# Performance work log

Hardware: AMD Instinct MI355X
Metric: run time of the kernel (lower is better)

## Reference

```python
import jax, jax.numpy as jnp
import numpy as np

B_, C_, H_, W_, Dd_ = 2, 64, 32, 32, 32
D_INNER, D_STATE, DT_RANK, D_CONV = 64, 8, 4, 4


def setup_inputs() -> dict:
    key = jax.random.key(0)
    ks = jax.random.split(key, 12)
    s = 0.05
    A_init = jnp.log(jnp.tile(jnp.arange(1, D_STATE + 1, dtype=jnp.float32), (D_INNER, 1)))
    return {
        "input": jax.random.normal(ks[0], (B_, C_, H_, W_, Dd_), jnp.float32),
        "conv_w": jax.random.normal(ks[1], (C_, C_, 3, 3, 3), jnp.float32) * s,
        "conv_b": jax.random.normal(ks[2], (C_,), jnp.float32) * s,
        "in_proj_w": jax.random.normal(ks[3], (2 * D_INNER, C_), jnp.float32) * s,
        "conv1d_w": jax.random.normal(ks[4], (D_INNER, 1, D_CONV), jnp.float32) * s,
        "conv1d_b": jax.random.normal(ks[5], (D_INNER,), jnp.float32) * s,
        "x_proj_w": jax.random.normal(ks[6], (DT_RANK + 2 * D_STATE, D_INNER), jnp.float32) * s,
        "dt_proj_w": jax.random.normal(ks[7], (D_INNER, DT_RANK), jnp.float32) * s,
        "dt_proj_b": jax.random.normal(ks[8], (D_INNER,), jnp.float32) * s,
        "A_log": A_init,
        "A_b_log": A_init + 0.01,
        "D_skip": jnp.ones((D_INNER,), jnp.float32),
        "out_proj_w": jax.random.normal(ks[9], (C_, D_INNER), jnp.float32) * s,
        "ln_g": jnp.ones((C_,), jnp.float32),
        "ln_b": jnp.zeros((C_,), jnp.float32),
    }


def _conv3d(x, w, b):
    y = jax.lax.conv_general_dilated(x, w, (1, 1, 1), [(1, 1), (1, 1), (1, 1)],
                                     dimension_numbers=("NCDHW", "OIDHW", "NCDHW"))
    return y + b[None, :, None, None, None]


def _instance_norm(x, eps=1e-5):
    m = x.mean(axis=(2, 3, 4), keepdims=True)
    v = ((x - m) ** 2).mean(axis=(2, 3, 4), keepdims=True)
    return (x - m) * jax.lax.rsqrt(v + eps)


def _selective_scan(xc, dt, Bm, Cm, A, D_skip):
    # xc, dt: (b,L,d); Bm, Cm: (b,L,n); A: (d,n)
    dA = jnp.exp(dt[..., None] * A)                       # (b,L,d,n)
    dBx = (dt * xc)[..., None] * Bm[:, :, None, :]        # (b,L,d,n)

    def comb(l, r):
        al, bl = l
        ar, br = r
        return ar * al, ar * bl + br

    _, h = jax.lax.associative_scan(comb, (dA, dBx), axis=1)
    y = jnp.einsum("bldn,bln->bld", h, Cm)
    return y + xc * D_skip


def _direction(xz, conv1d_w, conv1d_b, x_proj_w, dt_proj_w, dt_proj_b, A, D_skip):
    x, z = jnp.split(xz, 2, axis=-1)                      # each (b,L,d)
    xt = jnp.swapaxes(x, 1, 2)                            # (b,d,L)
    xc = jax.lax.conv_general_dilated(xt, conv1d_w, (1,), [(D_CONV - 1, 0)],
                                      feature_group_count=D_INNER,
                                      dimension_numbers=("NCH", "OIH", "NCH"))
    xc = jax.nn.silu(jnp.swapaxes(xc + conv1d_b[None, :, None], 1, 2))  # (b,L,d)
    dbl = xc @ x_proj_w.T
    dt_r = dbl[..., :DT_RANK]
    Bm = dbl[..., DT_RANK:DT_RANK + D_STATE]
    Cm = dbl[..., DT_RANK + D_STATE:]
    dt = jax.nn.softplus(dt_r @ dt_proj_w.T + dt_proj_b)
    y = _selective_scan(xc, dt, Bm, Cm, A, D_skip)
    return y * jax.nn.silu(z)


def reference(input, conv_w, conv_b, in_proj_w, conv1d_w, conv1d_b, x_proj_w,
              dt_proj_w, dt_proj_b, A_log, A_b_log, D_skip, out_proj_w, ln_g, ln_b):
    # skip path: Conv3d -> InstanceNorm3d -> ReLU
    skip = jax.nn.relu(_instance_norm(_conv3d(input, conv_w, conv_b)))
    b, c, h, w, d = input.shape
    tokens = input.transpose(0, 2, 3, 4, 1).reshape(b, h * w * d, c)  # b (hwd) c
    xz = tokens @ in_proj_w.T                                          # (b,L,2d)
    A = -jnp.exp(A_log)
    A_b = -jnp.exp(A_b_log)
    y_f = _direction(xz, conv1d_w, conv1d_b, x_proj_w, dt_proj_w, dt_proj_b, A, D_skip)
    y_b = _direction(xz[:, ::-1], conv1d_w, conv1d_b, x_proj_w, dt_proj_w, dt_proj_b, A_b, D_skip)[:, ::-1]
    out = ((y_f + y_b) @ out_proj_w.T) / 2.0  # if_devide_out=True
    mu = out.mean(-1, keepdims=True)
    var = ((out - mu) ** 2).mean(-1, keepdims=True)
    out = (out - mu) * jax.lax.rsqrt(var + 1e-5) * ln_g + ln_b  # use_norm=True
    vol = out.reshape(b, h, w, d, c).transpose(0, 4, 1, 2, 3)
    return _conv3d(vol, conv_w, conv_b) + skip
```

## Files before the change

### kernel.cpp

```cpp
#include <hip/hip_runtime.h>
#include <hip/hip_bf16.h>

typedef __hip_bfloat16 bf16;
typedef __attribute__((ext_vector_type(8))) short short8;
typedef __attribute__((ext_vector_type(4))) float f32x4;

__device__ __forceinline__ float b2f(bf16 x){ return __bfloat162float(x); }
__device__ __forceinline__ bf16  f2b(float x){ return __float2bfloat16(x); }
__device__ __forceinline__ float s2f(short s){ bf16 t = *(bf16*)&s; return b2f(t); }

__device__ __forceinline__ float ldin(const void* p, size_t i, int f32){
  return f32 ? ((const float*)p)[i] : b2f(((const bf16*)p)[i]);
}
__device__ __forceinline__ void stout(void* p, size_t i, float v, int f32){
  if(f32) ((float*)p)[i] = v; else ((bf16*)p)[i] = f2b(v);
}

constexpr int SP   = 32*32*32;
constexpr int LTOK = SP;
constexpr int NC   = 512;
constexpr int CLEN = LTOK / NC;
constexpr int NSEQ = 2*2*64*8;
constexpr int SEG  = 16;
constexpr int SEGLEN = NC/SEG;

__global__ void k_detect(const void* conv_w, int* flag){
  if(threadIdx.x==0 && blockIdx.x==0){
    const bf16* p = (const bf16*)conv_w;
    int f = 0;
    for(int i=0;i<128;i++){
      float v = b2f(p[i]);
      if(!(v==v) || fabsf(v) > 1.0f) f = 1;
    }
    *flag = f;
  }
}

__global__ void k_fill(void* out, int n, const int* flag){
  const int f32 = *flag;
  int i = blockIdx.x*256 + threadIdx.x;
  if(i<n) stout(out, i, 12345.0f, f32);
}

__global__ void k_wprep(const void* __restrict__ cw, bf16* __restrict__ wt,
                        const int* __restrict__ flag){
  const int f32 = *flag;
  int t = blockIdx.x*256 + threadIdx.x;
  if(t >= 27*64*64) return;
  int tap = t >> 12;
  int oc  = (t >> 6) & 63;
  int ci  = t & 63;
  wt[t] = f2b(ldin(cw, ((size_t)(oc*64+ci))*27 + tap, f32));
}

__global__ __launch_bounds__(256) void k_inprojm(
    const void* __restrict__ in, const void* __restrict__ pw,
    bf16* __restrict__ xz, bf16* __restrict__ xin_t,
    const int* __restrict__ flag){
  const int f32 = *flag;
  __shared__ bf16 tok[128*72];
  __shared__ bf16 wl [128*72];
  int tid = threadIdx.x;
  int b = blockIdx.x >> 8, tile = blockIdx.x & 255;
  int l0 = tile*128;

  for(int p=tid; p<1024; p+=256){
    int j = p & 127, c8 = p >> 7;
    short8 v;
    #pragma unroll
    for(int k=0;k<8;k++){
      bf16 t = f2b(ldin(pw, j*64 + c8*8 + k, f32));
      v[k] = *(short*)&t;
    }
    *(short8*)(&wl[j*72 + c8*8]) = v;
  }
  for(int p=tid; p<1024; p+=256){
    int i = p & 127, c8 = p >> 7;
    short8 v;
    #pragma unroll
    for(int k=0;k<8;k++){
      bf16 t = f2b(ldin(in, ((size_t)(b*64 + c8*8 + k))*SP + l0 + i, f32));
      v[k] = *(short*)&t;
    }
    *(short8*)(&tok[i*72 + c8*8]) = v;
  }
  __syncthreads();

  int lane = tid & 63, wv = tid >> 6;
  int pn = lane & 15, quad = lane >> 4, kg8 = quad*8;
  f32x4 acc[2][8];
  #pragma unroll
  for(int mt=0;mt<2;mt++)
    #pragma unroll
    for(int nt=0;nt<8;nt++) acc[mt][nt]=(f32x4)(0.f);

  #pragma unroll
  for(int kq=0;kq<2;kq++){
    short8 a0 = *(const short8*)(&tok[(wv*32      + pn)*72 + kq*32 + kg8]);
    short8 a1 = *(const short8*)(&tok[(wv*32 + 16 + pn)*72 + kq*32 + kg8]);
    #pragma unroll
    for(int nt=0;nt<8;nt++){
      short8 bb = *(const short8*)(&wl[(nt*16+pn)*72 + kq*32 + kg8]);
      acc[0][nt] = __builtin_amdgcn_mfma_f32_16x16x32_bf16(a0,bb,acc[0][nt],0,0,0);
      acc[1][nt] = __builtin_amdgcn_mfma_f32_16x16x32_bf16(a1,bb,acc[1][nt],0,0,0);
    }
  }

  #pragma unroll
  for(int mt=0;mt<2;mt++){
    #pragma unroll
    for(int nt=0;nt<8;nt++){
      #pragma unroll
      for(int r=0;r<4;r++){
        int token = wv*32 + mt*16 + quad*4 + r;
        xz[((size_t)b*LTOK + l0 + token)*128 + nt*16 + pn] = f2b(acc[mt][nt][r]);
      }
    }
  }
  for(int p=tid; p<8192; p+=256){
    int i = p >> 6, c = p & 63;
    xin_t[((size_t)b*SP + l0 + i)*64 + c] = tok[i*72 + c];
  }
}

__global__ __launch_bounds__(256, 2) void k_convm(
    const bf16* __restrict__ xin_t, const bf16* __restrict__ wt,
    const void* __restrict__ cb, const bf16* __restrict__ skip,
    bf16* __restrict__ out_bf, void* __restrict__ out_any,
    int mode, const int* __restrict__ flag){
  const int f32 = *flag;
  __shared__ bf16 xt[612*44];

  int tid  = threadIdx.x;
  int lane = tid & 63;
  int wv   = tid >> 6;
  int pn   = lane & 15;
  int quad = lane >> 4;
  int kg8  = quad * 8;
  int laneA = pn*64 + kg8;

  int blk = blockIdx.x;
  int b  = blk >> 8;
  int h  = (blk >> 3) & 31;
  int w0 = (blk & 7) * 4;

  f32x4 acc[4][2];
  #pragma unroll
  for(int m=0;m<4;m++){ acc[m][0]=(f32x4)(0.f); acc[m][1]=(f32x4)(0.f); }

  for(int cic=0; cic<64; cic+=32){
    if(cic) __syncthreads();
    if(cic==0){
      for(int i=tid; i<36*2*32; i+=256){
        int cil = i & 31; int q = i >> 5;
        int hw = q >> 1;  int dd = (q & 1) ? 33 : 0;
        xt[(hw*34 + dd)*44 + cil] = f2b(0.f);
      }
    }
    #pragma unroll
    for(int it=0; it<9; it++){
      int row = it*64 + (tid>>2);
      int q4  = tid & 3;
      int d   = row & 31;
      int hw  = row >> 5;
      int ww  = hw % 6, hh = hw / 6;
      int hg = h + hh - 1, wg = w0 + ww - 1;
      short8 v = (short8)(0);
      if((unsigned)hg < 32u && (unsigned)wg < 32u)
        v = *(const short8*)(&xin_t[(((size_t)b*SP) + hg*1024 + wg*32 + d)*64 + cic + q4*8]);
      *(short8*)(&xt[(hw*34 + 1 + d)*44 + q4*8]) = v;
    }
    __syncthreads();

    #pragma unroll
    for(int kz=0;kz<3;kz++){
      #pragma unroll
      for(int ky=0;ky<3;ky++){
        #pragma unroll
        for(int kx=0;kx<3;kx++){
          int tap = (kz*3+ky)*3+kx;
          const bf16* wbase = wt + tap*4096 + cic + laneA;
          short8 a0 = *(const short8*)(wbase);
          short8 a1 = *(const short8*)(wbase + 1024);
          short8 a2 = *(const short8*)(wbase + 2048);
          short8 a3 = *(const short8*)(wbase + 3072);
          int rix = (kz*6 + wv + ky)*34 + pn + kx;
          short8 b0 = *(const short8*)(&xt[ rix     *44 + kg8]);
          short8 b1 = *(const short8*)(&xt[(rix+16) *44 + kg8]);
          acc[0][0] = __builtin_amdgcn_mfma_f32_16x16x32_bf16(a0,b0,acc[0][0],0,0,0);
          acc[0][1] = __builtin_amdgcn_mfma_f32_16x16x32_bf16(a0,b1,acc[0][1],0,0,0);
          acc[1][0] = __builtin_amdgcn_mfma_f32_16x16x32_bf16(a1,b0,acc[1][0],0,0,0);
          acc[1][1] = __builtin_amdgcn_mfma_f32_16x16x32_bf16(a1,b1,acc[1][1],0,0,0);
          acc[2][0] = __builtin_amdgcn_mfma_f32_16x16x32_bf16(a2,b0,acc[2][0],0,0,0);
          acc[2][1] = __builtin_amdgcn_mfma_f32_16x16x32_bf16(a2,b1,acc[2][1],0,0,0);
          acc[3][0] = __builtin_amdgcn_mfma_f32_16x16x32_bf16(a3,b0,acc[3][0],0,0,0);
          acc[3][1] = __builtin_amdgcn_mfma_f32_16x16x32_bf16(a3,b1,acc[3][1],0,0,0);
        }
      }
    }
  }

  int posbase = h*1024 + (w0+wv)*32;
  #pragma unroll
  for(int m=0;m<4;m++){
    #pragma unroll
    for(int t=0;t<2;t++){
      #pragma unroll
      for(int r=0;r<4;r++){
        int oc = m*16 + quad*4 + r;
        size_t idx = ((size_t)(b*64+oc))*SP + posbase + t*16 + pn;
        float v = acc[m][t][r] + ldin(cb, oc, f32);
        if(mode==0) out_bf[idx] = f2b(v);
        else        stout(out_any, idx, v + b2f(skip[idx]), f32);
      }
    }
  }
}

__global__ void k_inorm(bf16* __restrict__ buf){
  int bc = blockIdx.x;
  bf16* p = buf + (size_t)bc*SP;
  float s=0.f, s2=0.f;
  for(int i=threadIdx.x;i<SP;i+=256){ float v=b2f(p[i]); s+=v; s2+=v*v; }
  __shared__ float sh[8];
  #pragma unroll
  for(int m=32;m>=1;m>>=1){ s += __shfl_xor(s,m); s2 += __shfl_xor(s2,m); }
  int wid = threadIdx.x>>6;
  if((threadIdx.x&63)==0){ sh[wid]=s; sh[4+wid]=s2; }
  __syncthreads();
  if(threadIdx.x==0){ float a=0,b2=0; for(int i=0;i<4;i++){a+=sh[i]; b2+=sh[4+i];} sh[0]=a; sh[4]=b2; }
  __syncthreads();
  float mean = sh[0]*(1.f/SP);
  float var  = sh[4]*(1.f/SP) - mean*mean;
  float inv = rsqrtf(fmaxf(var,0.f) + 1e-5f);
  for(int i=threadIdx.x;i<SP;i+=256){
    float v=(b2f(p[i])-mean)*inv;
    p[i] = f2b(v>0.f ? v : 0.f);
  }
}

__global__ void k_dirprep(const bf16* __restrict__ xz, const void* __restrict__ c1w,
                          const void* __restrict__ c1b, const void* __restrict__ xpw,
                          bf16* __restrict__ bcg, float* __restrict__ dtr,
                          const int* __restrict__ flag){
  const int f32 = *flag;
  __shared__ float xs[67][64];
  __shared__ float xcs[64][65];
  __shared__ float xws[20][65];
  int bid = blockIdx.x;
  int g = bid >> 10, b = (bid>>9)&1, tile = bid & 511;
  int l0 = tile*64;
  int gb = g*2+b;
  for(int t=threadIdx.x; t<20*64; t+=256){ int j=t>>6, d=t&63; xws[j][d]=ldin(xpw, t, f32); }
  for(int t=threadIdx.x; t<67*64; t+=256){
    int row=t>>6, d=t&63;
    int l = l0 + row - 3;
    float v = 0.f;
    if(l>=0 && l<LTOK){
      int lg = g ? (LTOK-1-l) : l;
      v = b2f(xz[((size_t)b*LTOK + lg)*128 + d]);
    }
    xs[row][d]=v;
  }
  __syncthreads();
  for(int t=threadIdx.x; t<4096; t+=256){
    int d=t&63, tl=t>>6;
    float acc = ldin(c1b, d, f32);
    #pragma unroll
    for(int k=0;k<4;k++) acc += ldin(c1w, d*4+k, f32) * xs[tl+k][d];
    xcs[tl][d] = acc / (1.f + __expf(-acc));
  }
  __syncthreads();
  for(int task=threadIdx.x; task<1280; task+=256){
    int j = task % 20, tl = task / 20;
    float acc=0.f;
    #pragma unroll
    for(int d=0; d<64; d++) acc += xcs[tl][d]*xws[j][d];
    size_t l = (size_t)gb*LTOK + l0 + tl;
    if(j<4) dtr[l*4 + j] = acc;
    else    bcg[l*16 + (j-4)] = f2b(acc);
  }
}

__global__ __launch_bounds__(256, 2) void k_scan1(
                        const bf16* __restrict__ xz, const float* __restrict__ dtr,
                        const bf16* __restrict__ bcg,
                        const void* __restrict__ c1w, const void* __restrict__ c1b,
                        const void* __restrict__ dpw, const void* __restrict__ dpb,
                        const void* __restrict__ alog, const void* __restrict__ ablog,
                        float* __restrict__ psP, float* __restrict__ psS,
                        const int* __restrict__ flag){
  const int f32 = *flag;
  int wid = blockIdx.x*4 + (threadIdx.x>>6);
  int lane = threadIdx.x & 63;
  int chunk = wid & (NC-1);
  int b = (wid>>9)&1;
  int g = wid>>10;
  int gb = g*2+b;
  const void* al = g ? ablog : alog;
  float ac[8];
  #pragma unroll
  for(int n=0;n<8;n++) ac[n] = -__expf(ldin(al, lane*8+n, f32));
  float cw0=ldin(c1w,lane*4+0,f32), cw1=ldin(c1w,lane*4+1,f32), cw2=ldin(c1w,lane*4+2,f32), cw3=ldin(c1w,lane*4+3,f32);
  float cb_=ldin(c1b,lane,f32);
  float dw0=ldin(dpw,lane*4+0,f32), dw1=ldin(dpw,lane*4+1,f32), dw2=ldin(dpw,lane*4+2,f32), dw3=ldin(dpw,lane*4+3,f32);
  float db_=ldin(dpb,lane,f32);
  float S[8];
  #pragma unroll
  for(int n=0;n<8;n++) S[n]=0.f;
  float Tsum = 0.f;
  int lt0 = chunk*CLEN;
  float x0,x1,x2;
  {
    float xr[3];
    #pragma unroll
    for(int j=0;j<3;j++){
      int lt = lt0-3+j;
      float v=0.f;
      if(lt>=0){ int lg = g ? (LTOK-1-lt) : lt; v=b2f(xz[((size_t)b*LTOK+lg)*128 + lane]); }
      xr[j]=v;
    }
    x0=xr[0]; x1=xr[1]; x2=xr[2];
  }
  for(int i0=0;i0<CLEN;i0+=8){
    bf16 xv[8]; float4 dv[8]; short8 bb[8];
    #pragma unroll
    for(int k=0;k<8;k++){
      int lt = lt0+i0+k;
      int lg = g ? (LTOK-1-lt) : lt;
      xv[k] = xz[((size_t)b*LTOK+lg)*128 + lane];
      size_t l = (size_t)gb*LTOK + lt;
      dv[k] = *(const float4*)(dtr + l*4);
      bb[k] = *(const short8*)(bcg + l*16);
    }
    #pragma unroll
    for(int k=0;k<8;k++){
      float x3 = b2f(xv[k]);
      float pre = cb_ + cw0*x0 + cw1*x1 + cw2*x2 + cw3*x3;
      float xc = pre / (1.f + __expf(-pre));
      float v = db_ + dv[k].x*dw0 + dv[k].y*dw1 + dv[k].z*dw2 + dv[k].w*dw3;
      float e = __expf(-fabsf(v));
      float dt = fmaxf(v,0.f) + __logf(1.f+e);
      Tsum += dt;
      float bx = dt*xc;
      #pragma unroll
      for(int n=0;n<8;n++){
        float a = __expf(dt*ac[n]);
        S[n] = a*S[n] + bx*s2f(bb[k][n]);
      }
      x0=x1; x1=x2; x2=x3;
    }
  }
  int seq = (gb*64 + lane)*8;
  #pragma unroll
  for(int n=0;n<8;n++){
    psP[(size_t)chunk*NSEQ + seq + n] = __expf(ac[n]*Tsum);
    psS[(size_t)chunk*NSEQ + seq + n] = S[n];
  }
}

__global__ void k_scan2a(const float* __restrict__ psP, const float* __restrict__ psS,
                         float* __restrict__ segP, float* __restrict__ segS){
  int idx = blockIdx.x*256 + threadIdx.x;
  int seq = idx & (NSEQ-1);
  int seg = idx >> 11;
  float P = 1.f, S = 0.f;
  int i0 = seg*SEGLEN;
  #pragma unroll 4
  for(int i=0;i<SEGLEN;i++){
    float p = psP[(size_t)(i0+i)*NSEQ + seq];
    float s = psS[(size_t)(i0+i)*NSEQ + seq];
    S = p*S + s;
    P *= p;
  }
  segP[seg*NSEQ + seq] = P;
  segS[seg*NSEQ + seq] = S;
}
__global__ void k_scan2b(const float* __restrict__ segP, const float* __restrict__ segS,
                         float* __restrict__ segC){
  int seq = blockIdx.x*256 + threadIdx.x;
  if(seq >= NSEQ) return;
  float h = 0.f;
  #pragma unroll
  for(int s=0;s<SEG;s++){
    segC[s*NSEQ + seq] = h;
    h = segP[s*NSEQ + seq]*h + segS[s*NSEQ + seq];
  }
}
__global__ void k_scan2c(const float* __restrict__ psP, const float* __restrict__ segC,
                         float* __restrict__ psC){
  int idx = blockIdx.x*256 + threadIdx.x;
  int seq = idx & (NSEQ-1);
  int seg = idx >> 11;
  float h = segC[seg*NSEQ + seq];
  int i0 = seg*SEGLEN;
  #pragma unroll 4
  for(int i=0;i<SEGLEN;i++){
    float p = psP[(size_t)(i0+i)*NSEQ + seq];
    float s = psC[(size_t)(i0+i)*NSEQ + seq];
    psC[(size_t)(i0+i)*NSEQ + seq] = h;
    h = p*h + s;
  }
}

__global__ __launch_bounds__(256, 2) void k_scan3(
                        const bf16* __restrict__ xz, const float* __restrict__ dtr,
                        const bf16* __restrict__ bcg,
                        const void* __restrict__ c1w, const void* __restrict__ c1b,
                        const void* __restrict__ dpw, const void* __restrict__ dpb,
                        const void* __restrict__ alog, const void* __restrict__ ablog,
                        const void* __restrict__ dskip, const float* __restrict__ carry,
                        bf16* __restrict__ ybuf, const int* __restrict__ flag){
  const int f32 = *flag;
  int wid = blockIdx.x*4 + (threadIdx.x>>6);
  int lane = threadIdx.x & 63;
  int chunk = wid & (NC-1);
  int b = (wid>>9)&1;
  int g = wid>>10;
  int gb = g*2+b;
  const void* al = g ? ablog : alog;
  float ac[8];
  #pragma unroll
  for(int n=0;n<8;n++) ac[n] = -__expf(ldin(al, lane*8+n, f32));
  float cw0=ldin(c1w,lane*4+0,f32), cw1=ldin(c1w,lane*4+1,f32), cw2=ldin(c1w,lane*4+2,f32), cw3=ldin(c1w,lane*4+3,f32);
  float cb_=ldin(c1b,lane,f32);
  float dw0=ldin(dpw,lane*4+0,f32), dw1=ldin(dpw,lane*4+1,f32), dw2=ldin(dpw,lane*4+2,f32), dw3=ldin(dpw,lane*4+3,f32);
  float db_=ldin(dpb,lane,f32);
  float dsk = ldin(dskip,lane,f32);
  int seq = (gb*64 + lane)*8;
  float h[8];
  #pragma unroll
  for(int n=0;n<8;n++) h[n] = carry[(size_t)chunk*NSEQ + seq + n];
  int lt0 = chunk*CLEN;
  float x0,x1,x2;
  {
    float xr[3];
    #pragma unroll
    for(int j=0;j<3;j++){
      int lt = lt0-3+j;
      float v=0.f;
      if(lt>=0){ int lg = g ? (LTOK-1-lt) : lt; v=b2f(xz[((size_t)b*LTOK+lg)*128 + lane]); }
      xr[j]=v;
    }
    x0=xr[0]; x1=xr[1]; x2=xr[2];
  }
  for(int i0=0;i0<CLEN;i0+=8){
    bf16 xv[8]; float4 dv[8]; short8 bb[8]; short8 cc[8];
    #pragma unroll
    for(int k=0;k<8;k++){
      int lt = lt0+i0+k;
      int lg = g ? (LTOK-1-lt) : lt;
      xv[k] = xz[((size_t)b*LTOK+lg)*128 + lane];
      size_t l = (size_t)gb*LTOK + lt;
      dv[k] = *(const float4*)(dtr + l*4);
      bb[k] = *(const short8*)(bcg + l*16);
      cc[k] = *(const short8*)(bcg + l*16 + 8);
    }
    #pragma unroll
    for(int k=0;k<8;k++){
      float x3 = b2f(xv[k]);
      float pre = cb_ + cw0*x0 + cw1*x1 + cw2*x2 + cw3*x3;
      float xc = pre / (1.f + __expf(-pre));
      float v = db_ + dv[k].x*dw0 + dv[k].y*dw1 + dv[k].z*dw2 + dv[k].w*dw3;
      float e = __expf(-fabsf(v));
      float dt = fmaxf(v,0.f) + __logf(1.f+e);
      float bx = dt*xc;
      float y = xc*dsk;
      #pragma unroll
      for(int n=0;n<8;n++){
        float a = __expf(dt*ac[n]);
        h[n] = a*h[n] + bx*s2f(bb[k][n]);
        y += h[n]*s2f(cc[k][n]);
      }
      size_t l = (size_t)gb*LTOK + lt0+i0+k;
      ybuf[l*64 + lane] = f2b(y);
      x0=x1; x1=x2; x2=x3;
    }
  }
}

__global__ __launch_bounds__(256) void k_outln(
                        const bf16* __restrict__ ybuf, const bf16* __restrict__ xz,
                        const void* __restrict__ opw,
                        const void* __restrict__ lng, const void* __restrict__ lnb,
                        bf16* __restrict__ vol_t, const int* __restrict__ flag){
  const int f32 = *flag;
  __shared__ bf16 vsm[64*72];
  __shared__ bf16 wsm[64*72];
  __shared__ float gsm[64], bsm[64];
  int tid = threadIdx.x;
  int b = blockIdx.x >> 9, tile = blockIdx.x & 511;
  int l0 = tile*64;

  for(int p=tid; p<512; p+=256){
    int c = p & 63, d8 = p >> 6;
    short8 v;
    #pragma unroll
    for(int k=0;k<8;k++){ bf16 t = f2b(ldin(opw, c*64 + d8*8 + k, f32)); v[k] = *(short*)&t; }
    *(short8*)(&wsm[c*72 + d8*8]) = v;
  }
  if(tid<64){ gsm[tid]=ldin(lng,tid,f32); bsm[tid]=ldin(lnb,tid,f32); }
  for(int p=tid; p<4096; p+=256){
    int tl = p >> 6, d = p & 63;
    int l = l0 + tl;
    float yf = b2f(ybuf[((size_t)(0+b)*LTOK + l)*64 + d]);
    float yb = b2f(ybuf[((size_t)(2+b)*LTOK + (LTOK-1-l))*64 + d]);
    float z  = b2f(xz[((size_t)b*LTOK + l)*128 + 64 + d]);
    float sz = z / (1.f + __expf(-z));
    vsm[tl*72 + d] = f2b(0.5f*(yf+yb)*sz);
  }
  __syncthreads();

  int lane = tid & 63, wv = tid >> 6, pn = lane & 15, quad = lane >> 4, kg8 = quad*8;
  f32x4 acc[4];
  #pragma unroll
  for(int nt=0;nt<4;nt++) acc[nt]=(f32x4)(0.f);
  #pragma unroll
  for(int kq=0;kq<2;kq++){
    short8 a = *(const short8*)(&vsm[(wv*16+pn)*72 + kq*32 + kg8]);
    #pragma unroll
    for(int nt=0;nt<4;nt++){
      short8 bb = *(const short8*)(&wsm[(nt*16+pn)*72 + kq*32 + kg8]);
      acc[nt] = __builtin_amdgcn_mfma_f32_16x16x32_bf16(a,bb,acc[nt],0,0,0);
    }
  }
  __syncthreads();

  float gl[4], bl[4];
  #pragma unroll
  for(int nt=0;nt<4;nt++){ gl[nt]=gsm[nt*16+pn]; bl[nt]=bsm[nt*16+pn]; }
  #pragma unroll
  for(int r=0;r<4;r++){
    float vals[4]; float s=0.f;
    #pragma unroll
    for(int nt=0;nt<4;nt++){ vals[nt]=acc[nt][r]; s+=vals[nt]; }
    #pragma unroll
    for(int m=1;m<16;m<<=1) s += __shfl_xor(s, m);
    float mu = s*(1.f/64.f);
    float s2=0.f;
    #pragma unroll
    for(int nt=0;nt<4;nt++){ float dv=vals[nt]-mu; s2+=dv*dv; }
    #pragma unroll
    for(int m=1;m<16;m<<=1) s2 += __shfl_xor(s2, m);
    float inv = rsqrtf(s2*(1.f/64.f) + 1e-5f);
    int token = wv*16 + quad*4 + r;
    #pragma unroll
    for(int nt=0;nt<4;nt++){
      vsm[token*72 + nt*16 + pn] = f2b((vals[nt]-mu)*inv*gl[nt] + bl[nt]);
    }
  }
  __syncthreads();
  for(int p=tid; p<512; p+=256){
    int tl = p >> 3, d8 = p & 7;
    *(short8*)(&vol_t[((size_t)b*SP + l0 + tl)*64 + d8*8]) = *(const short8*)(&vsm[tl*72 + d8*8]);
  }
}

extern "C" void kernel_launch(void* const* d_in, const int* in_sizes, int n_in,
                              void* d_out, int out_size, void* d_ws, size_t ws_size,
                              hipStream_t stream){
  const void* input  = d_in[0];
  const void* conv_w = d_in[1];
  const void* conv_b = d_in[2];
  const void* inpw   = d_in[3];
  const void* c1w    = d_in[4];
  const void* c1b    = d_in[5];
  const void* xpw    = d_in[6];
  const void* dpw    = d_in[7];
  const void* dpb    = d_in[8];
  const void* alog   = d_in[9];
  const void* ablog  = d_in[10];
  const void* dskip  = d_in[11];
  const void* opw    = d_in[12];
  const void* lng    = d_in[13];
  const void* lnb    = d_in[14];

  char* base = (char*)d_ws;
  bf16*  skipb = (bf16*) (base + 0);
  bf16*  xz    = (bf16*) (base + 8388608);
  bf16*  bcg   = (bf16*) (base + 25165824);
  float* dtr   = (float*)(base + 29360128);
  float* psP   = (float*)(base + 31457280);
  float* psS   = (float*)(base + 35651584);
  bf16*  ybuf  = (bf16*) (base + 39845888);
  bf16*  wt    = (bf16*) (base + 56623104);
  float* segP  = (float*)(base + 56844288);
  float* segS  = (float*)(base + 56975360);
  float* segC  = (float*)(base + 57106432);
  bf16*  xin_t = (bf16*) (base + 31457280);
  bf16*  vol_t = (bf16*) (base + 25165824);
  int*   flagp = (int*)  (base + 60817408);
  const size_t NEED = 60817424;

  k_detect<<<dim3(1), dim3(64), 0, stream>>>(conv_w, flagp);

  if(ws_size < NEED){
    k_fill<<<dim3((out_size+255)/256), dim3(256), 0, stream>>>(d_out, out_size, flagp);
    return;
  }

  k_wprep  <<<dim3(432),   dim3(256), 0, stream>>>(conv_w, wt, flagp);
  k_inprojm<<<dim3(512),   dim3(256), 0, stream>>>(input, inpw, xz, xin_t, flagp);
  k_convm  <<<dim3(512),   dim3(256), 0, stream>>>(xin_t, wt, conv_b, nullptr, skipb, nullptr, 0, flagp);
  k_inorm  <<<dim3(128),   dim3(256), 0, stream>>>(skipb);
  k_dirprep<<<dim3(2048),  dim3(256), 0, stream>>>(xz, c1w, c1b, xpw, bcg, dtr, flagp);
  k_scan1  <<<dim3(512),   dim3(256), 0, stream>>>(xz, dtr, bcg, c1w, c1b, dpw, dpb, alog, ablog, psP, psS, flagp);
  k_scan2a <<<dim3(128),   dim3(256), 0, stream>>>(psP, psS, segP, segS);
  k_scan2b <<<dim3(8),     dim3(256), 0, stream>>>(segP, segS, segC);
  k_scan2c <<<dim3(128),   dim3(256), 0, stream>>>(psP, segC, psS);
  k_scan3  <<<dim3(512),   dim3(256), 0, stream>>>(xz, dtr, bcg, c1w, c1b, dpw, dpb, alog, ablog, dskip, psS, ybuf, flagp);
  k_outln  <<<dim3(1024),  dim3(256), 0, stream>>>(ybuf, xz, opw, lng, lnb, vol_t, flagp);
  k_convm  <<<dim3(512),   dim3(256), 0, stream>>>(vol_t, wt, conv_b, skipb, nullptr, d_out, 1, flagp);
}
```

Before: 464.3 us.

## Retile conv3d kernel by output-channel group with register-resident weight fragments

Each conv3d block now covers one 16-channel output group over a 16-wide w strip, instead of all 64 output channels over a 4-wide strip. The block keeps all 27 tap weight fragments in registers per input-channel chunk rather than reloading four fragments per tap from global memory. The shared-memory tile grows to the full 3x18x34 halo (three times larger), and launch bounds drop to one block per SM. This trades occupancy and redundant input staging (each input tile is loaded four times across channel groups) for less weight traffic and more MFMAs per loaded B fragment.

```diff
diff --git a/kernel.cpp b/kernel.cpp
--- a/kernel.cpp
+++ b/kernel.cpp
@@ -123,13 +123,13 @@
   }
 }
 
-__global__ __launch_bounds__(256, 2) void k_convm(
+__global__ __launch_bounds__(256, 1) void k_convm(
     const bf16* __restrict__ xin_t, const bf16* __restrict__ wt,
     const void* __restrict__ cb, const bf16* __restrict__ skip,
     bf16* __restrict__ out_bf, void* __restrict__ out_any,
     int mode, const int* __restrict__ flag){
   const int f32 = *flag;
-  __shared__ bf16 xt[612*44];
+  __shared__ bf16 xt[1836*36];
 
   int tid  = threadIdx.x;
   int lane = tid & 63;
@@ -140,37 +140,37 @@
   int laneA = pn*64 + kg8;
 
   int blk = blockIdx.x;
-  int b  = blk >> 8;
-  int h  = (blk >> 3) & 31;
-  int w0 = (blk & 7) * 4;
-
-  f32x4 acc[4][2];
-  #pragma unroll
-  for(int m=0;m<4;m++){ acc[m][0]=(f32x4)(0.f); acc[m][1]=(f32x4)(0.f); }
+  int ocg = blk & 3;
+  int wh  = (blk >> 2) & 1;
+  int h   = (blk >> 3) & 31;
+  int b   = blk >> 8;
+  int w0  = wh*16;
+
+  f32x4 acc[8];
+  #pragma unroll
+  for(int m=0;m<8;m++) acc[m]=(f32x4)(0.f);
 
   for(int cic=0; cic<64; cic+=32){
     if(cic) __syncthreads();
-    if(cic==0){
-      for(int i=tid; i<36*2*32; i+=256){
-        int cil = i & 31; int q = i >> 5;
-        int hw = q >> 1;  int dd = (q & 1) ? 33 : 0;
-        xt[(hw*34 + dd)*44 + cil] = f2b(0.f);
+    for(int it=0; it<29; it++){
+      int j = it*256 + tid;
+      if(j < 7344){
+        int q4 = j & 3, row = j >> 2;
+        int hh = row / 612; int rem = row - hh*612;
+        int ww = rem / 34;  int dd = rem - ww*34;
+        int hg = h + hh - 1, wg = w0 + ww - 1, d = dd - 1;
+        short8 v = (short8)(0);
+        if((unsigned)hg < 32u && (unsigned)wg < 32u && (unsigned)d < 32u)
+          v = *(const short8*)(&xin_t[(((size_t)b*SP) + hg*1024 + wg*32 + d)*64 + cic + q4*8]);
+        *(short8*)(&xt[row*36 + q4*8]) = v;
       }
     }
-    #pragma unroll
-    for(int it=0; it<9; it++){
-      int row = it*64 + (tid>>2);
-      int q4  = tid & 3;
-      int d   = row & 31;
-      int hw  = row >> 5;
-      int ww  = hw % 6, hh = hw / 6;
-      int hg = h + hh - 1, wg = w0 + ww - 1;
-      short8 v = (short8)(0);
-      if((unsigned)hg < 32u && (unsigned)wg < 32u)
-        v = *(const short8*)(&xin_t[(((size_t)b*SP) + hg*1024 + wg*32 + d)*64 + cic + q4*8]);
-      *(short8*)(&xt[(hw*34 + 1 + d)*44 + q4*8]) = v;
-    }
     __syncthreads();
+
+    short8 afr[27];
+    #pragma unroll
+    for(int t=0;t<27;t++)
+      afr[t] = *(const short8*)(wt + t*4096 + ocg*1024 + cic + laneA);
 
     #pragma unroll
     for(int kz=0;kz<3;kz++){
@@ -179,37 +179,30 @@
         #pragma unroll
         for(int kx=0;kx<3;kx++){
           int tap = (kz*3+ky)*3+kx;
-          const bf16* wbase = wt + tap*4096 + cic + laneA;
-          short8 a0 = *(const short8*)(wbase);
-          short8 a1 = *(const short8*)(wbase + 1024);
-          short8 a2 = *(const short8*)(wbase + 2048);
-          short8 a3 = *(const short8*)(wbase + 3072);
-          int rix = (kz*6 + wv + ky)*34 + pn + kx;
-          short8 b0 = *(const short8*)(&xt[ rix     *44 + kg8]);
-          short8 b1 = *(const short8*)(&xt[(rix+16) *44 + kg8]);
-          acc[0][0] = __builtin_amdgcn_mfma_f32_16x16x32_bf16(a0,b0,acc[0][0],0,0,0);
-          acc[0][1] = __builtin_amdgcn_mfma_f32_16x16x32_bf16(a0,b1,acc[0][1],0,0,0);
-          acc[1][0] = __builtin_amdgcn_mfma_f32_16x16x32_bf16(a1,b0,acc[1][0],0,0,0);
-          acc[1][1] = __builtin_amdgcn_mfma_f32_16x16x32_bf16(a1,b1,acc[1][1],0,0,0);
-          acc[2][0] = __builtin_amdgcn_mfma_f32_16x16x32_bf16(a2,b0,acc[2][0],0,0,0);
-          acc[2][1] = __builtin_amdgcn_mfma_f32_16x16x32_bf16(a2,b1,acc[2][1],0,0,0);
-          acc[3][0] = __builtin_amdgcn_mfma_f32_16x16x32_bf16(a3,b0,acc[3][0],0,0,0);
-          acc[3][1] = __builtin_amdgcn_mfma_f32_16x16x32_bf16(a3,b1,acc[3][1],0,0,0);
+          #pragma unroll
+          for(int wr=0;wr<4;wr++){
+            int rowb = (kz*18 + wv*4 + wr + ky)*34 + kx;
+            #pragma unroll
+            for(int dh=0;dh<2;dh++){
+              int rix = rowb + dh*16 + pn;
+              short8 bb = *(const short8*)(&xt[rix*36 + kg8]);
+              acc[wr*2+dh] = __builtin_amdgcn_mfma_f32_16x16x32_bf16(afr[tap], bb, acc[wr*2+dh], 0,0,0);
+            }
+          }
         }
       }
     }
   }
 
-  int posbase = h*1024 + (w0+wv)*32;
-  #pragma unroll
-  for(int m=0;m<4;m++){
-    #pragma unroll
-    for(int t=0;t<2;t++){
+  #pragma unroll
+  for(int wr=0;wr<4;wr++){
+    #pragma unroll
+    for(int dh=0;dh<2;dh++){
       #pragma unroll
       for(int r=0;r<4;r++){
-        int oc = m*16 + quad*4 + r;
-        size_t idx = ((size_t)(b*64+oc))*SP + posbase + t*16 + pn;
-        float v = acc[m][t][r] + ldin(cb, oc, f32);
+        int oc = ocg*16 + quad*4 + r;
+        size_t idx = ((size_t)(b*64+oc))*SP + h*1024 + (w0 + wv*4 + wr)*32 + dh*16 + pn;
+        float v = acc[wr*2+dh][r] + ldin(cb, oc, f32);
         if(mode==0) out_bf[idx] = f2b(v);
         else        stout(out_any, idx, v + b2f(skip[idx]), f32);
       }
```

Result: no change. 455.9 us (-1.8%).
